# Kernel tuning notes

Hardware: AMD Instinct MI355X
Metric: run time of the kernel (lower is better)

## Reference

```python
import jax, jax.numpy as jnp
import numpy as np

N_NODES = 100000
N_EDGES = 3200000
NUM_FEATURES = 256
HIDDEN = 16
NUM_CLASSES = 40


def gcn_conv(x, edge_index, W, b, num_nodes):
    """PyG GCNConv: linear -> add self-loops -> symmetric deg norm -> scatter-add -> bias."""
    x = x @ W  # [N, out]
    loop = jnp.arange(num_nodes)
    src = jnp.concatenate([edge_index[0], loop])  # messages flow src -> dst
    dst = jnp.concatenate([edge_index[1], loop])
    # degree of target nodes (with self-loops)
    deg = jax.ops.segment_sum(jnp.ones_like(dst, dtype=x.dtype), dst,
                              num_segments=num_nodes)
    dinv = jnp.where(deg > 0, jax.lax.rsqrt(deg), 0.0)
    norm = dinv[src] * dinv[dst]  # [E+N]
    out = jax.ops.segment_sum(x[src] * norm[:, None], dst,
                              num_segments=num_nodes)
    return out + b


def setup_inputs() -> dict:
    key = jax.random.key(0)
    k1, k2, k3, k4 = jax.random.split(key, 4)
    x = jax.random.normal(k1, (N_NODES, NUM_FEATURES), dtype=jnp.float32)
    edge_index = jax.random.randint(k2, (2, N_EDGES), 0, N_NODES, dtype=jnp.int64)
    W1 = jax.random.normal(k3, (NUM_FEATURES, HIDDEN), dtype=jnp.float32) / np.sqrt(NUM_FEATURES)
    b1 = jnp.zeros((HIDDEN,), dtype=jnp.float32)
    W2 = jax.random.normal(k4, (HIDDEN, NUM_CLASSES), dtype=jnp.float32) / np.sqrt(HIDDEN)
    b2 = jnp.zeros((NUM_CLASSES,), dtype=jnp.float32)
    return {"x": x, "edge_index": edge_index, "W1": W1, "b1": b1, "W2": W2, "b2": b2}


def reference(x, edge_index, W1, b1, W2, b2):
    h = jax.nn.relu(gcn_conv(x, edge_index, W1, b1, N_NODES))
    return gcn_conv(h, edge_index, W2, b2, N_NODES)
```

## Files before the change

kernel.cpp:

```cpp
#include <hip/hip_runtime.h>
#include <hip/hip_fp16.h>

#define N_NODES   100000
#define N_EDGES   3200000
#define F_IN      256
#define HID       16
#define NCLS      40

#define CHUNK     16384
#define NBLK      ((N_EDGES + CHUNK - 1) / CHUNK)
#define B2SHIFT   9
#define NB2       ((N_NODES + 511) >> B2SHIFT)
#define BCAP      17408

__global__ __launch_bounds__(256) void hist_kernel(const int* __restrict__ ei,
                                                   int* __restrict__ hist_blk) {
    __shared__ int h[NB2];
    int blk = blockIdx.x, t = threadIdx.x;
    for (int i = t; i < NB2; i += 256) h[i] = 0;
    __syncthreads();
    int e0 = blk * CHUNK;
    int eN = min(CHUNK, N_EDGES - e0);
    for (int i = t; i < eN; i += 256)
        atomicAdd(&h[ei[N_EDGES + e0 + i] >> B2SHIFT], 1);
    __syncthreads();
    for (int i = t; i < NB2; i += 256) hist_blk[i * NBLK + blk] = h[i];
}

__global__ __launch_bounds__(256) void rowscan_kernel(int* __restrict__ hist_blk,
                                                      int* __restrict__ rowsum) {
    __shared__ int part[256];
    int b = blockIdx.x, t = threadIdx.x;
    int v = (t < NBLK) ? hist_blk[b * NBLK + t] : 0;
    part[t] = v;
    __syncthreads();
    for (int off = 1; off < 256; off <<= 1) {
        int u = (t >= off) ? part[t - off] : 0;
        __syncthreads();
        part[t] += u;
        __syncthreads();
    }
    if (t < NBLK) hist_blk[b * NBLK + t] = part[t] - v;
    if (t == 255) rowsum[b] = part[255];
}

__global__ __launch_bounds__(256) void basescan_kernel(const int* __restrict__ rowsum,
                                                       int* __restrict__ bucket_base) {
    __shared__ int part[256];
    int t = threadIdx.x;
    int v = (t < NB2) ? rowsum[t] : 0;
    part[t] = v;
    __syncthreads();
    for (int off = 1; off < 256; off <<= 1) {
        int u = (t >= off) ? part[t - off] : 0;
        __syncthreads();
        part[t] += u;
        __syncthreads();
    }
    if (t < NB2) bucket_base[t] = part[t] - v;
}

__global__ __launch_bounds__(256) void bin2_kernel(const int* __restrict__ ei,
                                                   const int* __restrict__ hist_blk,
                                                   const int* __restrict__ bucket_base,
                                                   int* __restrict__ buf) {
    __shared__ int cur[NB2];
    int blk = blockIdx.x, t = threadIdx.x;
    for (int i = t; i < NB2; i += 256)
        cur[i] = bucket_base[i] + hist_blk[i * NBLK + blk];
    __syncthreads();
    int e0 = blk * CHUNK;
    int eN = min(CHUNK, N_EDGES - e0);
    for (int i = t; i < eN; i += 256) {
        int d = ei[N_EDGES + e0 + i];
        int s = ei[e0 + i];
        int pos = atomicAdd(&cur[d >> B2SHIFT], 1);
        buf[pos] = ((d & 511) << 17) | s;
    }
}

__global__ __launch_bounds__(512) void build_kernel(const int* __restrict__ buf,
                                                    const int* __restrict__ bucket_base,
                                                    const int* __restrict__ rowsum,
                                                    int* __restrict__ rowptr,
                                                    float* __restrict__ dinv,
                                                    int* __restrict__ csr_src) {
    __shared__ int lbuf[BCAP];
    __shared__ int hist[512], offs[512], cur[512];
    int b = blockIdx.x, t = threadIdx.x;
    int base = bucket_base[b];
    int cnt  = rowsum[b];
    hist[t] = 0;
    __syncthreads();
    for (int i = t; i < cnt; i += 512) {
        int v = buf[base + i];
        if (i < BCAP) lbuf[i] = v;
        atomicAdd(&hist[v >> 17], 1);
    }
    __syncthreads();
    int v = hist[t];
    offs[t] = v;
    __syncthreads();
    for (int off = 1; off < 512; off <<= 1) {
        int u = (t >= off) ? offs[t - off] : 0;
        __syncthreads();
        offs[t] += u;
        __syncthreads();
    }
    int ex = offs[t] - v;
    int n = (b << B2SHIFT) + t;
    if (n < N_NODES) {
        rowptr[n] = base + ex;
        dinv[n]   = rsqrtf((float)(v + 1));
    }
    if (b == 0 && t == 0) rowptr[N_NODES] = N_EDGES;
    cur[t] = ex;
    __syncthreads();
    for (int i = t; i < cnt; i += 512) {
        int p = (i < BCAP) ? lbuf[i] : buf[base + i];
        int pos = atomicAdd(&cur[p >> 17], 1);
        csr_src[base + pos] = p & 0x1FFFF;
    }
}

__global__ __launch_bounds__(256) void gemm1_kernel(const float* __restrict__ x,
                                                    const float* __restrict__ W1,
                                                    const float* __restrict__ dinv,
                                                    __half* __restrict__ y1h) {
    __shared__ float W1s[F_IN * HID];
    int t = threadIdx.x;
    #pragma unroll
    for (int i = 0; i < (F_IN * HID) / 256; i++) W1s[t + i * 256] = W1[t + i * 256];
    __syncthreads();

    int n = blockIdx.x * 256 + t;
    if (n >= N_NODES) return;

    const float4* xr = (const float4*)(x + (size_t)n * F_IN);
    float acc[HID];
    #pragma unroll
    for (int h = 0; h < HID; h++) acc[h] = 0.f;

    #pragma unroll 4
    for (int k4 = 0; k4 < F_IN / 4; k4++) {
        float4 xv = xr[k4];
        int k = k4 * 4;
        #pragma unroll
        for (int h = 0; h < HID; h++) {
            acc[h] += xv.x * W1s[(k + 0) * HID + h] + xv.y * W1s[(k + 1) * HID + h]
                    + xv.z * W1s[(k + 2) * HID + h] + xv.w * W1s[(k + 3) * HID + h];
        }
    }
    float dv = dinv[n];
    __half2 hp[8];
    #pragma unroll
    for (int j = 0; j < 8; j++)
        hp[j] = __float22half2_rn(make_float2(acc[2 * j] * dv, acc[2 * j + 1] * dv));
    float4* o = (float4*)(y1h + (size_t)n * HID);
    o[0] = ((float4*)hp)[0];
    o[1] = ((float4*)hp)[1];
}

__device__ __forceinline__ void acc_row(const float4* __restrict__ tab, int s, float* acc) {
    float4 v0 = tab[(size_t)s * 2 + 0];
    float4 v1 = tab[(size_t)s * 2 + 1];
    const __half2* a0 = (const __half2*)&v0;
    const __half2* a1 = (const __half2*)&v1;
    #pragma unroll
    for (int j = 0; j < 4; j++) {
        float2 f0 = __half22float2(a0[j]);
        float2 f1 = __half22float2(a1[j]);
        acc[2 * j]         += f0.x;
        acc[2 * j + 1]     += f0.y;
        acc[8 + 2 * j]     += f1.x;
        acc[8 + 2 * j + 1] += f1.y;
    }
}

__global__ __launch_bounds__(256) void gather1_kernel(const int* __restrict__ rowptr,
                                                      const int* __restrict__ csr_src,
                                                      const __half* __restrict__ y1h,
                                                      const float* __restrict__ b1,
                                                      const float* __restrict__ dinv,
                                                      __half* __restrict__ zh) {
    int n   = blockIdx.x * 16 + (threadIdx.x >> 4);
    int sub = threadIdx.x & 15;
    const float4* tab = (const float4*)y1h;
    int beg = rowptr[n], end = rowptr[n + 1];
    float acc[16];
    #pragma unroll
    for (int i = 0; i < 16; i++) acc[i] = 0.f;
    if (sub == 0) acc_row(tab, n, acc);
    for (int e = beg + sub; e < end; e += 16)
        acc_row(tab, csr_src[e], acc);
    #pragma unroll
    for (int m = 1; m < 16; m <<= 1) {
        #pragma unroll
        for (int i = 0; i < 16; i++) acc[i] += __shfl_xor(acc[i], m, 16);
    }
    if (sub < 2) {
        float dv = dinv[n];
        const float4* b1q = (const float4*)b1;
        float4 ba = b1q[sub * 2], bb = b1q[sub * 2 + 1];
        const float* bp = (sub == 0) ? (const float*)&ba : (const float*)&ba;
        float bv[8] = {ba.x, ba.y, ba.z, ba.w, bb.x, bb.y, bb.z, bb.w};
        (void)bp;
        __half2 outp[4];
        #pragma unroll
        for (int j = 0; j < 4; j++) {
            float2 r;
            r.x = fmaxf(dv * acc[sub * 8 + 2 * j]     + bv[2 * j],     0.f) * dv;
            r.y = fmaxf(dv * acc[sub * 8 + 2 * j + 1] + bv[2 * j + 1], 0.f) * dv;
            outp[j] = __float22half2_rn(r);
        }
        *(float4*)(zh + (size_t)n * HID + sub * 8) = *(float4*)outp;
    }
}

__global__ __launch_bounds__(256) void gather2_kernel(const int* __restrict__ rowptr,
                                                      const int* __restrict__ csr_src,
                                                      const __half* __restrict__ zh,
                                                      const float* __restrict__ W2,
                                                      const float* __restrict__ b2,
                                                      const float* __restrict__ dinv,
                                                      float* __restrict__ out) {
    __shared__ float W2s[HID * NCLS];
    __shared__ float b2s[NCLS];
    int t = threadIdx.x;
    for (int i = t; i < HID * NCLS; i += 256) W2s[i] = W2[i];
    if (t < NCLS) b2s[t] = b2[t];
    __syncthreads();

    int n   = blockIdx.x * 16 + (t >> 4);
    int sub = t & 15;
    const float4* tab = (const float4*)zh;
    int beg = rowptr[n], end = rowptr[n + 1];
    float acc[16];
    #pragma unroll
    for (int i = 0; i < 16; i++) acc[i] = 0.f;
    if (sub == 0) acc_row(tab, n, acc);
    for (int e = beg + sub; e < end; e += 16)
        acc_row(tab, csr_src[e], acc);
    #pragma unroll
    for (int m = 1; m < 16; m <<= 1) {
        #pragma unroll
        for (int i = 0; i < 16; i++) acc[i] += __shfl_xor(acc[i], m, 16);
    }
    if (sub < 10) {
        float dv = dinv[n];
        int c0 = sub * 4;
        float o0 = 0.f, o1 = 0.f, o2 = 0.f, o3 = 0.f;
        #pragma unroll
        for (int h = 0; h < HID; h++) {
            float a = acc[h];
            const float* w = &W2s[h * NCLS + c0];
            o0 += a * w[0]; o1 += a * w[1]; o2 += a * w[2]; o3 += a * w[3];
        }
        float4 r = make_float4(dv * o0 + b2s[c0],     dv * o1 + b2s[c0 + 1],
                               dv * o2 + b2s[c0 + 2], dv * o3 + b2s[c0 + 3]);
        *(float4*)(out + (size_t)n * NCLS + c0) = r;
    }
}

extern "C" void kernel_launch(void* const* d_in, const int* in_sizes, int n_in,
                              void* d_out, int out_size, void* d_ws, size_t ws_size,
                              hipStream_t stream) {
    const float* x   = (const float*)d_in[0];
    const int*   ei  = (const int*)  d_in[1];
    const float* W1  = (const float*)d_in[2];
    const float* b1  = (const float*)d_in[3];
    const float* W2  = (const float*)d_in[4];
    const float* b2  = (const float*)d_in[5];
    float* out = (float*)d_out;

    char* ws = (char*)d_ws;
    size_t off = 0;
    int*   hist_blk    = (int*)(ws + off); off += (size_t)NB2 * NBLK * 4;
    int*   rowsum      = (int*)(ws + off); off += (size_t)NB2 * 4;
    int*   bucket_base = (int*)(ws + off); off += (size_t)NB2 * 4;
    off = (off + 15) & ~(size_t)15;
    int*    rowptr  = (int*)   (ws + off); off += (size_t)(N_NODES + 1) * 4;
    off = (off + 15) & ~(size_t)15;
    float*  dinv    = (float*) (ws + off); off += (size_t)N_NODES * 4;
    int*    csr_src = (int*)   (ws + off); off += (size_t)N_EDGES * 4;
    int*    buf     = (int*)   (ws + off); off += (size_t)N_EDGES * 4;
    __half* y1h     = (__half*)(ws + off); off += (size_t)N_NODES * HID * 2;
    __half* zh      = (__half*)(ws + off); off += (size_t)N_NODES * HID * 2;

    hist_kernel    <<<NBLK, 256, 0, stream>>>(ei, hist_blk);
    rowscan_kernel <<<NB2, 256, 0, stream>>>(hist_blk, rowsum);
    basescan_kernel<<<1, 256, 0, stream>>>(rowsum, bucket_base);
    bin2_kernel    <<<NBLK, 256, 0, stream>>>(ei, hist_blk, bucket_base, buf);
    build_kernel   <<<NB2, 512, 0, stream>>>(buf, bucket_base, rowsum, rowptr, dinv, csr_src);

    gemm1_kernel  <<<(N_NODES + 255) / 256, 256, 0, stream>>>(x, W1, dinv, y1h);
    gather1_kernel<<<N_NODES / 16, 256, 0, stream>>>(rowptr, csr_src, y1h, b1, dinv, zh);
    gather2_kernel<<<N_NODES / 16, 256, 0, stream>>>(rowptr, csr_src, zh, W2, b2, dinv, out);
}
```

Measured before the change: 357.9 us.

## Replace CSR build and row gathers with bucketed shared-memory atomic aggregation

Drops the per-bucket CSR sort (rowptr/csr_src build) and aggregates straight from the destination-binned edge buffer. Buckets shrink to 128 nodes, and each block sums neighbour features into a shared-memory accumulator using float atomics. A small kernel now computes per-node degree and dinv from the bucket contents. This removes a full pass that reads and writes the 3.2M-edge arrays. In exchange it performs 16 LDS atomics per edge per layer, may hit bank conflicts, runs only about 780 blocks, and sums in a nondeterministic order.

```diff
diff --git a/kernel.cpp b/kernel.cpp
--- a/kernel.cpp
+++ b/kernel.cpp
@@ -9,9 +9,9 @@
 
 #define CHUNK     16384
 #define NBLK      ((N_EDGES + CHUNK - 1) / CHUNK)
-#define B2SHIFT   9
-#define NB2       ((N_NODES + 511) >> B2SHIFT)
-#define BCAP      17408
+#define B2SHIFT   7
+#define BNODES    128
+#define NB2       ((N_NODES + BNODES - 1) >> B2SHIFT)
 
 __global__ __launch_bounds__(256) void hist_kernel(const int* __restrict__ ei,
                                                    int* __restrict__ hist_blk) {
@@ -44,14 +44,14 @@
     if (t == 255) rowsum[b] = part[255];
 }
 
-__global__ __launch_bounds__(256) void basescan_kernel(const int* __restrict__ rowsum,
-                                                       int* __restrict__ bucket_base) {
-    __shared__ int part[256];
+__global__ __launch_bounds__(1024) void basescan_kernel(const int* __restrict__ rowsum,
+                                                        int* __restrict__ bucket_base) {
+    __shared__ int part[1024];
     int t = threadIdx.x;
     int v = (t < NB2) ? rowsum[t] : 0;
     part[t] = v;
     __syncthreads();
-    for (int off = 1; off < 256; off <<= 1) {
+    for (int off = 1; off < 1024; off <<= 1) {
         int u = (t >= off) ? part[t - off] : 0;
         __syncthreads();
         part[t] += u;
@@ -75,52 +75,25 @@
         int d = ei[N_EDGES + e0 + i];
         int s = ei[e0 + i];
         int pos = atomicAdd(&cur[d >> B2SHIFT], 1);
-        buf[pos] = ((d & 511) << 17) | s;
-    }
-}
-
-__global__ __launch_bounds__(512) void build_kernel(const int* __restrict__ buf,
-                                                    const int* __restrict__ bucket_base,
-                                                    const int* __restrict__ rowsum,
-                                                    int* __restrict__ rowptr,
-                                                    float* __restrict__ dinv,
-                                                    int* __restrict__ csr_src) {
-    __shared__ int lbuf[BCAP];
-    __shared__ int hist[512], offs[512], cur[512];
-    int b = blockIdx.x, t = threadIdx.x;
-    int base = bucket_base[b];
-    int cnt  = rowsum[b];
-    hist[t] = 0;
-    __syncthreads();
-    for (int i = t; i < cnt; i += 512) {
-        int v = buf[base + i];
-        if (i < BCAP) lbuf[i] = v;
-        atomicAdd(&hist[v >> 17], 1);
-    }
-    __syncthreads();
-    int v = hist[t];
-    offs[t] = v;
-    __syncthreads();
-    for (int off = 1; off < 512; off <<= 1) {
-        int u = (t >= off) ? offs[t - off] : 0;
-        __syncthreads();
-        offs[t] += u;
-        __syncthreads();
-    }
-    int ex = offs[t] - v;
+        buf[pos] = ((d & (BNODES - 1)) << 17) | s;
+    }
+}
+
+__global__ __launch_bounds__(256) void dinv_kernel(const int* __restrict__ buf,
+                                                   const int* __restrict__ bucket_base,
+                                                   const int* __restrict__ rowsum,
+                                                   float* __restrict__ dinv) {
+    __shared__ int cnt[BNODES];
+    int b = blockIdx.x, t = threadIdx.x;
+    if (t < BNODES) cnt[t] = 0;
+    __syncthreads();
+    int base = bucket_base[b], c = rowsum[b];
+    for (int i = t; i < c; i += 256)
+        atomicAdd(&cnt[buf[base + i] >> 17], 1);
+    __syncthreads();
     int n = (b << B2SHIFT) + t;
-    if (n < N_NODES) {
-        rowptr[n] = base + ex;
-        dinv[n]   = rsqrtf((float)(v + 1));
-    }
-    if (b == 0 && t == 0) rowptr[N_NODES] = N_EDGES;
-    cur[t] = ex;
-    __syncthreads();
-    for (int i = t; i < cnt; i += 512) {
-        int p = (i < BCAP) ? lbuf[i] : buf[base + i];
-        int pos = atomicAdd(&cur[p >> 17], 1);
-        csr_src[base + pos] = p & 0x1FFFF;
-    }
+    if (t < BNODES && n < N_NODES)
+        dinv[n] = rsqrtf((float)(cnt[t] + 1));
 }
 
 __global__ __launch_bounds__(256) void gemm1_kernel(const float* __restrict__ x,
@@ -161,104 +134,122 @@
     o[1] = ((float4*)hp)[1];
 }
 
-__device__ __forceinline__ void acc_row(const float4* __restrict__ tab, int s, float* acc) {
-    float4 v0 = tab[(size_t)s * 2 + 0];
-    float4 v1 = tab[(size_t)s * 2 + 1];
-    const __half2* a0 = (const __half2*)&v0;
-    const __half2* a1 = (const __half2*)&v1;
-    #pragma unroll
-    for (int j = 0; j < 4; j++) {
-        float2 f0 = __half22float2(a0[j]);
-        float2 f1 = __half22float2(a1[j]);
-        acc[2 * j]         += f0.x;
-        acc[2 * j + 1]     += f0.y;
-        acc[8 + 2 * j]     += f1.x;
-        acc[8 + 2 * j + 1] += f1.y;
-    }
-}
-
-__global__ __launch_bounds__(256) void gather1_kernel(const int* __restrict__ rowptr,
-                                                      const int* __restrict__ csr_src,
-                                                      const __half* __restrict__ y1h,
-                                                      const float* __restrict__ b1,
-                                                      const float* __restrict__ dinv,
-                                                      __half* __restrict__ zh) {
-    int n   = blockIdx.x * 16 + (threadIdx.x >> 4);
-    int sub = threadIdx.x & 15;
+__global__ __launch_bounds__(256) void agg1_kernel(const int* __restrict__ buf,
+                                                   const int* __restrict__ bucket_base,
+                                                   const int* __restrict__ rowsum,
+                                                   const __half* __restrict__ y1h,
+                                                   const float* __restrict__ b1,
+                                                   const float* __restrict__ dinv,
+                                                   __half* __restrict__ zh) {
+    __shared__ float accs[HID * BNODES];
+    int b = blockIdx.x, t = threadIdx.x;
+    for (int i = t; i < HID * BNODES; i += 256) accs[i] = 0.f;
+    __syncthreads();
+    int base = bucket_base[b], c = rowsum[b];
     const float4* tab = (const float4*)y1h;
-    int beg = rowptr[n], end = rowptr[n + 1];
-    float acc[16];
-    #pragma unroll
-    for (int i = 0; i < 16; i++) acc[i] = 0.f;
-    if (sub == 0) acc_row(tab, n, acc);
-    for (int e = beg + sub; e < end; e += 16)
-        acc_row(tab, csr_src[e], acc);
-    #pragma unroll
-    for (int m = 1; m < 16; m <<= 1) {
-        #pragma unroll
-        for (int i = 0; i < 16; i++) acc[i] += __shfl_xor(acc[i], m, 16);
-    }
-    if (sub < 2) {
+    for (int i = t; i < c; i += 256) {
+        int p = buf[base + i];
+        int ld = p >> 17, s = p & 0x1FFFF;
+        float4 v0 = tab[(size_t)s * 2 + 0];
+        float4 v1 = tab[(size_t)s * 2 + 1];
+        const __half2* a0 = (const __half2*)&v0;
+        const __half2* a1 = (const __half2*)&v1;
+        #pragma unroll
+        for (int j = 0; j < 4; j++) {
+            float2 f0 = __half22float2(a0[j]);
+            float2 f1 = __half22float2(a1[j]);
+            atomicAdd(&accs[(2 * j)     * BNODES + ld], f0.x);
+            atomicAdd(&accs[(2 * j + 1) * BNODES + ld], f0.y);
+            atomicAdd(&accs[(8 + 2 * j)     * BNODES + ld], f1.x);
+            atomicAdd(&accs[(8 + 2 * j + 1) * BNODES + ld], f1.y);
+        }
+    }
+    __syncthreads();
+    int ld = t >> 1, q = t & 1;
+    int n = (b << B2SHIFT) + ld;
+    if (n < N_NODES) {
         float dv = dinv[n];
-        const float4* b1q = (const float4*)b1;
-        float4 ba = b1q[sub * 2], bb = b1q[sub * 2 + 1];
-        const float* bp = (sub == 0) ? (const float*)&ba : (const float*)&ba;
-        float bv[8] = {ba.x, ba.y, ba.z, ba.w, bb.x, bb.y, bb.z, bb.w};
-        (void)bp;
+        float4 sv = tab[(size_t)n * 2 + q];
+        const __half2* ap = (const __half2*)&sv;
         __half2 outp[4];
         #pragma unroll
         for (int j = 0; j < 4; j++) {
+            float2 f = __half22float2(ap[j]);
+            int f0 = q * 8 + 2 * j, f1 = f0 + 1;
+            float s0 = accs[f0 * BNODES + ld] + f.x;
+            float s1 = accs[f1 * BNODES + ld] + f.y;
             float2 r;
-            r.x = fmaxf(dv * acc[sub * 8 + 2 * j]     + bv[2 * j],     0.f) * dv;
-            r.y = fmaxf(dv * acc[sub * 8 + 2 * j + 1] + bv[2 * j + 1], 0.f) * dv;
+            r.x = fmaxf(dv * s0 + b1[f0], 0.f) * dv;
+            r.y = fmaxf(dv * s1 + b1[f1], 0.f) * dv;
             outp[j] = __float22half2_rn(r);
         }
-        *(float4*)(zh + (size_t)n * HID + sub * 8) = *(float4*)outp;
-    }
-}
-
-__global__ __launch_bounds__(256) void gather2_kernel(const int* __restrict__ rowptr,
-                                                      const int* __restrict__ csr_src,
-                                                      const __half* __restrict__ zh,
-                                                      const float* __restrict__ W2,
-                                                      const float* __restrict__ b2,
-                                                      const float* __restrict__ dinv,
-                                                      float* __restrict__ out) {
+        *(float4*)(zh + (size_t)n * HID + q * 8) = *(float4*)outp;
+    }
+}
+
+__global__ __launch_bounds__(256) void agg2_kernel(const int* __restrict__ buf,
+                                                   const int* __restrict__ bucket_base,
+                                                   const int* __restrict__ rowsum,
+                                                   const __half* __restrict__ zh,
+                                                   const float* __restrict__ W2,
+                                                   const float* __restrict__ b2,
+                                                   const float* __restrict__ dinv,
+                                                   float* __restrict__ out) {
+    __shared__ float accs[HID * BNODES];
     __shared__ float W2s[HID * NCLS];
     __shared__ float b2s[NCLS];
-    int t = threadIdx.x;
+    int b = blockIdx.x, t = threadIdx.x;
     for (int i = t; i < HID * NCLS; i += 256) W2s[i] = W2[i];
     if (t < NCLS) b2s[t] = b2[t];
-    __syncthreads();
-
-    int n   = blockIdx.x * 16 + (t >> 4);
-    int sub = t & 15;
+    for (int i = t; i < HID * BNODES; i += 256) accs[i] = 0.f;
+    __syncthreads();
+    int base = bucket_base[b], c = rowsum[b];
     const float4* tab = (const float4*)zh;
-    int beg = rowptr[n], end = rowptr[n + 1];
-    float acc[16];
-    #pragma unroll
-    for (int i = 0; i < 16; i++) acc[i] = 0.f;
-    if (sub == 0) acc_row(tab, n, acc);
-    for (int e = beg + sub; e < end; e += 16)
-        acc_row(tab, csr_src[e], acc);
-    #pragma unroll
-    for (int m = 1; m < 16; m <<= 1) {
-        #pragma unroll
-        for (int i = 0; i < 16; i++) acc[i] += __shfl_xor(acc[i], m, 16);
-    }
-    if (sub < 10) {
-        float dv = dinv[n];
-        int c0 = sub * 4;
-        float o0 = 0.f, o1 = 0.f, o2 = 0.f, o3 = 0.f;
-        #pragma unroll
-        for (int h = 0; h < HID; h++) {
-            float a = acc[h];
-            const float* w = &W2s[h * NCLS + c0];
-            o0 += a * w[0]; o1 += a * w[1]; o2 += a * w[2]; o3 += a * w[3];
-        }
-        float4 r = make_float4(dv * o0 + b2s[c0],     dv * o1 + b2s[c0 + 1],
-                               dv * o2 + b2s[c0 + 2], dv * o3 + b2s[c0 + 3]);
-        *(float4*)(out + (size_t)n * NCLS + c0) = r;
+    for (int i = t; i < c; i += 256) {
+        int p = buf[base + i];
+        int ld = p >> 17, s = p & 0x1FFFF;
+        float4 v0 = tab[(size_t)s * 2 + 0];
+        float4 v1 = tab[(size_t)s * 2 + 1];
+        const __half2* a0 = (const __half2*)&v0;
+        const __half2* a1 = (const __half2*)&v1;
+        #pragma unroll
+        for (int j = 0; j < 4; j++) {
+            float2 f0 = __half22float2(a0[j]);
+            float2 f1 = __half22float2(a1[j]);
+            atomicAdd(&accs[(2 * j)     * BNODES + ld], f0.x);
+            atomicAdd(&accs[(2 * j + 1) * BNODES + ld], f0.y);
+            atomicAdd(&accs[(8 + 2 * j)     * BNODES + ld], f1.x);
+            atomicAdd(&accs[(8 + 2 * j + 1) * BNODES + ld], f1.y);
+        }
+    }
+    __syncthreads();
+    {
+        int ld = t >> 1, q = t & 1;
+        int n = (b << B2SHIFT) + ld;
+        if (n < N_NODES) {
+            float4 sv = tab[(size_t)n * 2 + q];
+            const __half2* ap = (const __half2*)&sv;
+            #pragma unroll
+            for (int j = 0; j < 4; j++) {
+                float2 f = __half22float2(ap[j]);
+                accs[(q * 8 + 2 * j)     * BNODES + ld] += f.x;
+                accs[(q * 8 + 2 * j + 1) * BNODES + ld] += f.y;
+            }
+        }
+    }
+    __syncthreads();
+    int n0 = b << B2SHIFT;
+    for (int idx = t; idx < BNODES * NCLS; idx += 256) {
+        int ld = idx / NCLS, cc = idx - ld * NCLS;
+        int n = n0 + ld;
+        if (n < N_NODES) {
+            float dv = dinv[n];
+            float s = 0.f;
+            #pragma unroll
+            for (int h = 0; h < HID; h++)
+                s += accs[h * BNODES + ld] * W2s[h * NCLS + cc];
+            out[(size_t)n * NCLS + cc] = dv * s + b2s[cc];
+        }
     }
 }
 
@@ -279,21 +270,18 @@
     int*   rowsum      = (int*)(ws + off); off += (size_t)NB2 * 4;
     int*   bucket_base = (int*)(ws + off); off += (size_t)NB2 * 4;
     off = (off + 15) & ~(size_t)15;
-    int*    rowptr  = (int*)   (ws + off); off += (size_t)(N_NODES + 1) * 4;
-    off = (off + 15) & ~(size_t)15;
-    float*  dinv    = (float*) (ws + off); off += (size_t)N_NODES * 4;
-    int*    csr_src = (int*)   (ws + off); off += (size_t)N_EDGES * 4;
-    int*    buf     = (int*)   (ws + off); off += (size_t)N_EDGES * 4;
-    __half* y1h     = (__half*)(ws + off); off += (size_t)N_NODES * HID * 2;
-    __half* zh      = (__half*)(ws + off); off += (size_t)N_NODES * HID * 2;
+    float*  dinv = (float*) (ws + off); off += (size_t)N_NODES * 4;
+    int*    buf  = (int*)   (ws + off); off += (size_t)N_EDGES * 4;
+    __half* y1h  = (__half*)(ws + off); off += (size_t)N_NODES * HID * 2;
+    __half* zh   = (__half*)(ws + off); off += (size_t)N_NODES * HID * 2;
 
     hist_kernel    <<<NBLK, 256, 0, stream>>>(ei, hist_blk);
     rowscan_kernel <<<NB2, 256, 0, stream>>>(hist_blk, rowsum);
-    basescan_kernel<<<1, 256, 0, stream>>>(rowsum, bucket_base);
+    basescan_kernel<<<1, 1024, 0, stream>>>(rowsum, bucket_base);
     bin2_kernel    <<<NBLK, 256, 0, stream>>>(ei, hist_blk, bucket_base, buf);
-    build_kernel   <<<NB2, 512, 0, stream>>>(buf, bucket_base, rowsum, rowptr, dinv, csr_src);
-
-    gemm1_kernel  <<<(N_NODES + 255) / 256, 256, 0, stream>>>(x, W1, dinv, y1h);
-    gather1_kernel<<<N_NODES / 16, 256, 0, stream>>>(rowptr, csr_src, y1h, b1, dinv, zh);
-    gather2_kernel<<<N_NODES / 16, 256, 0, stream>>>(rowptr, csr_src, zh, W2, b2, dinv, out);
-}
+    dinv_kernel    <<<NB2, 256, 0, stream>>>(buf, bucket_base, rowsum, dinv);
+
+    gemm1_kernel<<<(N_NODES + 255) / 256, 256, 0, stream>>>(x, W1, dinv, y1h);
+    agg1_kernel <<<NB2, 256, 0, stream>>>(buf, bucket_base, rowsum, y1h, b1, dinv, zh);
+    agg2_kernel <<<NB2, 256, 0, stream>>>(buf, bucket_base, rowsum, zh, W2, b2, dinv, out);
+}
```

Result: slower. 969.3 us (+170.8%).
